# Performance work log

Measured on AMD Instinct MI355X. Metric: run time of the kernel, lower is better.

Reference implementation:

```python
import jax, jax.numpy as jnp
import numpy as np

V, E, H, C, M, CLS = 32000, 300, 512, 256, 512, 1
B, T = 64, 128
NEG = -1e9


def setup_inputs() -> dict:
    key = jax.random.key(0)
    ks = jax.random.split(key, 16)
    u = lambda k, shape, r: jax.random.uniform(k, shape, jnp.float32, -r, r)
    klstm = 1.0 / np.sqrt(H)
    inp = {
        "s1": jax.random.randint(ks[0], (B, T), 0, V, dtype=jnp.int32),
        "s2": jax.random.randint(ks[1], (B, T), 0, V, dtype=jnp.int32),
        "s1_length": jax.random.randint(ks[2], (B,), 1, T + 1, dtype=jnp.int32),
        "s2_length": jax.random.randint(ks[3], (B,), 1, T + 1, dtype=jnp.int32),
        "s1_h0": jnp.zeros((2, B, H), jnp.float32),
        "s1_c0": jnp.zeros((2, B, H), jnp.float32),
        "s2_h0": jnp.zeros((2, B, H), jnp.float32),
        "s2_c0": jnp.zeros((2, B, H), jnp.float32),
        "emb": jax.random.normal(ks[4], (V, E), jnp.float32) * 0.1,
        "Wih_f": u(ks[5], (4 * H, E), klstm),
        "Whh_f": u(ks[6], (4 * H, H), klstm),
        "b_f": u(ks[7], (4 * H,), klstm),
        "Wih_b": u(ks[8], (4 * H, E), klstm),
        "Whh_b": u(ks[9], (4 * H, H), klstm),
        "b_b": u(ks[10], (4 * H,), klstm),
        "S1W": u(ks[11], (C, 2 * H), 0.1),
        "S2W": u(ks[12], (1, C), 0.1),
        "mlpW": u(ks[13], (M, 4 * H), 0.1),
        "mlpb": jnp.zeros((M,), jnp.float32),
        "outW": u(ks[14], (CLS, M), 0.1),
        "outb": jnp.zeros((CLS,), jnp.float32),
    }
    return inp


def lstm(x, h0, c0, Wih, Whh, b):
    # x: [B,T,E] -> outputs [B,T,H]; PyTorch gate order i,f,g,o
    xW = jnp.einsum("bte,ge->btg", x, Wih) + b  # [B,T,4H]

    def step(carry, xw):
        h, c = carry
        g = xw + h @ Whh.T
        i, f, gg, o = jnp.split(g, 4, axis=-1)
        c = jax.nn.sigmoid(f) * c + jax.nn.sigmoid(i) * jnp.tanh(gg)
        h = jax.nn.sigmoid(o) * jnp.tanh(c)
        return (h, c), h

    _, hs = jax.lax.scan(step, (h0, c0), jnp.swapaxes(xW, 0, 1))
    return jnp.swapaxes(hs, 0, 1)


def encode(tokens, lens, h0, c0, emb, Wih_f, Whh_f, b_f, Wih_b, Whh_b, b_b, S1W, S2W):
    x = emb[tokens]  # [B,T,E]
    t = jnp.arange(tokens.shape[1])
    # reverse-within-valid-length indices (pack/pad semantics for bwd direction)
    idx = jnp.where(t[None, :] < lens[:, None], lens[:, None] - 1 - t[None, :], t[None, :])
    out_f = lstm(x, h0[0], c0[0], Wih_f, Whh_f, b_f)
    x_rev = jnp.take_along_axis(x, idx[:, :, None], axis=1)
    out_b = lstm(x_rev, h0[1], c0[1], Wih_b, Whh_b, b_b)
    out_b = jnp.take_along_axis(out_b, idx[:, :, None], axis=1)
    Hout = jnp.concatenate([out_f, out_b], axis=-1)  # [B,T,2H]
    # attention pooling: S2(tanh(S1(H))), softmax over valid positions
    scores = jnp.einsum("btc,c->bt", jnp.tanh(jnp.einsum("btd,cd->btc", Hout, S1W)), S2W[0])
    scores = jnp.where(t[None, :] < lens[:, None], scores, NEG)
    attn = jax.nn.softmax(scores, axis=1)
    return jnp.einsum("bt,btd->bd", attn, Hout)  # [B,2H]


def reference(s1, s2, s1_length, s2_length, s1_h0, s1_c0, s2_h0, s2_c0, emb,
              Wih_f, Whh_f, b_f, Wih_b, Whh_b, b_b, S1W, S2W, mlpW, mlpb, outW, outb):
    r1 = encode(s1, s1_length, s1_h0, s1_c0, emb, Wih_f, Whh_f, b_f, Wih_b, Whh_b, b_b, S1W, S2W)
    r2 = encode(s2, s2_length, s2_h0, s2_c0, emb, Wih_f, Whh_f, b_f, Wih_b, Whh_b, b_b, S1W, S2W)
    merged = jnp.concatenate([r1 + r2, (r1 - r2) ** 2], axis=1)  # [B,4H]
    out_mlp = merged @ mlpW.T + mlpb  # no activation, per original
    return jax.nn.sigmoid(out_mlp @ outW.T + outb)  # [B,CLS]
```

## Files before the change

kernel.cpp:

```cpp
#include <hip/hip_runtime.h>
#include <hip/hip_bf16.h>

#define B_  64
#define T_  128
#define E_  300
#define EP  320
#define H_  512
#define G4  2048
#define R_  128
#define C_  256
#define M_  512
#define TS  (T_ + 1)
#define NB  128
#define SENT 0xFFFFFFFFFFFFFFFFULL

typedef short bf16x8 __attribute__((ext_vector_type(8)));
typedef float f32x4  __attribute__((ext_vector_type(4)));
#define MFMA(a, b, c) __builtin_amdgcn_mfma_f32_16x16x32_bf16((a), (b), (c), 0, 0, 0)

__device__ __forceinline__ float fsig(float x) { return 1.0f / (1.0f + __expf(-x)); }
__device__ __forceinline__ float ftanh(float x) {
    float a = fminf(fabsf(x), 15.0f);
    float e = __expf(2.0f * a);
    return copysignf((e - 1.0f) / (e + 1.0f), x);
}
__device__ __forceinline__ ushort f2bf(float f) {
    __hip_bfloat16 h = __float2bfloat16(f);
    return *reinterpret_cast<ushort*>(&h);
}
__device__ __forceinline__ float bf2f(ushort u) {
    __hip_bfloat16 h = *reinterpret_cast<__hip_bfloat16*>(&u);
    return __bfloat162float(h);
}

__global__ __launch_bounds__(256) void k_cvt_all(
    const float* __restrict__ emb,
    const float* __restrict__ Wih_f, const float* __restrict__ Wih_b,
    const float* __restrict__ Whh_f, const float* __restrict__ Whh_b,
    const float* __restrict__ S1W,
    const float* __restrict__ s1_h0, const float* __restrict__ s2_h0,
    ushort* __restrict__ embB,
    ushort* __restrict__ WihBf, ushort* __restrict__ WihBb,
    ushort* __restrict__ WhhBf, ushort* __restrict__ WhhBb,
    ushort* __restrict__ S1WB,
    ushort* __restrict__ hfB, ushort* __restrict__ hbB)
{
    int b = blockIdx.x;
    if (b >= 40448) {
        const int r = b - 40448;
        const int rl = (r < B_) ? r : r - B_;
        const float* h0 = (r < B_) ? s1_h0 : s2_h0;
        for (int j = threadIdx.x; j < H_; j += 256) {
            hfB[(long)r * TS * H_ + j] = f2bf(h0[(long)0 * B_ * H_ + (long)rl * H_ + j]);
            hbB[(long)r * TS * H_ + j] = f2bf(h0[(long)1 * B_ * H_ + (long)rl * H_ + j]);
        }
        return;
    }
    const float* src; ushort* dst; int r, sk, dk;
    if (b < 32000)      { src = emb;   dst = embB;  r = b;          sk = E_;    dk = EP; }
    else if (b < 34048) { src = Wih_f; dst = WihBf; r = b - 32000;  sk = E_;    dk = EP; }
    else if (b < 36096) { src = Wih_b; dst = WihBb; r = b - 34048;  sk = E_;    dk = EP; }
    else if (b < 38144) { src = Whh_f; dst = WhhBf; r = b - 36096;  sk = H_;    dk = H_; }
    else if (b < 40192) { src = Whh_b; dst = WhhBb; r = b - 38144;  sk = H_;    dk = H_; }
    else                { src = S1W;   dst = S1WB;  r = b - 40192;  sk = 2*H_;  dk = 2*H_; }
    for (int c = threadIdx.x; c < dk; c += 256)
        dst[(long)r * dk + c] = (c < sk) ? f2bf(src[(long)r * sk + c]) : (ushort)0;
}

__global__ __launch_bounds__(256) void k_embed_mfma(
    const int* __restrict__ s1, const int* __restrict__ s2,
    const int* __restrict__ l1, const int* __restrict__ l2,
    const ushort* __restrict__ embB,
    const ushort* __restrict__ WihBf, const ushort* __restrict__ WihBb,
    const float* __restrict__ b_f, const float* __restrict__ b_b,
    ushort* __restrict__ xf, ushort* __restrict__ xb)
{
    const int dir = blockIdx.z;
    const int r   = blockIdx.y >> 1;
    const int t0  = (blockIdx.y & 1) * 64;
    const int N0  = blockIdx.x * 128;
    const int L   = (r < B_) ? l1[r] : l2[r - B_];
    if (L <= t0) return;

    const int tid = threadIdx.x;
    const int lane = tid & 63, w = tid >> 6;
    const int wm = w & 1, wn = w >> 1;
    const int l15 = lane & 15, q8 = (lane >> 4) * 8;

    __shared__ int toks[64];
    __shared__ __align__(16) ushort As[64][40];
    __shared__ __align__(16) ushort Bs[128][40];

    if (tid < 64) {
        int t  = t0 + tid;
        int tt = dir ? ((t < L) ? (L - 1 - t) : t) : t;
        toks[tid] = (r < B_) ? s1[r * T_ + tt] : s2[(r - B_) * T_ + tt];
    }
    __syncthreads();

    const ushort* Wih  = dir ? WihBb : WihBf;
    const float*  bias = dir ? b_b : b_f;

    f32x4 acc[2][4] = {};

    for (int k0 = 0; k0 < EP; k0 += 32) {
        {
            int row = tid >> 2, seg = tid & 3;
            *(uint4*)&As[row][seg * 8] =
                *(const uint4*)&embB[(long)toks[row] * EP + k0 + seg * 8];
        }
#pragma unroll
        for (int p = 0; p < 2; ++p) {
            int u = tid + p * 256;
            int row = u >> 2, seg = u & 3;
            *(uint4*)&Bs[row][seg * 8] =
                *(const uint4*)&Wih[(long)(N0 + row) * EP + k0 + seg * 8];
        }
        __syncthreads();
        bf16x8 af[2], bfr[4];
#pragma unroll
        for (int mt = 0; mt < 2; ++mt)
            af[mt] = *(const bf16x8*)&As[wm * 32 + mt * 16 + l15][q8];
#pragma unroll
        for (int nt = 0; nt < 4; ++nt)
            bfr[nt] = *(const bf16x8*)&Bs[wn * 64 + nt * 16 + l15][q8];
#pragma unroll
        for (int mt = 0; mt < 2; ++mt)
#pragma unroll
            for (int nt = 0; nt < 4; ++nt)
                acc[mt][nt] = MFMA(af[mt], bfr[nt], acc[mt][nt]);
        __syncthreads();
    }

    ushort* xout = dir ? xb : xf;
#pragma unroll
    for (int mt = 0; mt < 2; ++mt) {
        int m = r * T_ + t0 + wm * 32 + mt * 16 + (lane >> 4) * 4;
#pragma unroll
        for (int nt = 0; nt < 4; ++nt) {
            int col = N0 + wn * 64 + nt * 16 + l15;
            float bv = bias[col];
#pragma unroll
            for (int rg = 0; rg < 4; ++rg) {
                uint v = f2bf(acc[mt][nt][rg] + bv);
                uint pv = (uint)__shfl_xor((int)v, 1);
                if (!(lane & 1))
                    *(uint*)&xout[(long)(m + rg) * G4 + col] = v | (pv << 16);
            }
        }
    }
}

__global__ __launch_bounds__(256) void k_recur(
    const ushort* __restrict__ xf, const ushort* __restrict__ xb,
    ushort* __restrict__ hfB, ushort* __restrict__ hbB,
    const ushort* __restrict__ WhhBf, const ushort* __restrict__ WhhBb,
    const float* __restrict__ s1_c0, const float* __restrict__ s2_c0)
{
    const int bx = blockIdx.x;
    const int s  = bx >> 6;
    const int rb = (bx >> 4) & 3;
    const int jb = bx & 15;
    const int r0 = rb * 32, j0 = jb * 32;

    const ushort* xW  = s ? xb : xf;
    const ushort* Whh = s ? WhhBb : WhhBf;
    ushort* hB = s ? hbB : hfB;

    const int tid = threadIdx.x;
    const int lane = tid & 63;
    const int g = tid >> 6;
    const int l15 = lane & 15, q8 = (lane >> 4) * 8;

    __shared__ __align__(16) ushort As[32][520];
    __shared__ float Gs[4][32][33];

    bf16x8 bfr[2][16];
#pragma unroll
    for (int nt = 0; nt < 2; ++nt) {
        const ushort* brow = &Whh[((long)g * H_ + j0 + nt * 16 + l15) * H_];
#pragma unroll
        for (int ks = 0; ks < 16; ++ks)
            bfr[nt][ks] = *(const bf16x8*)&brow[ks * 32 + q8];
    }

    const int rr = tid >> 3, jj = (tid & 7) * 4;
    const int rg_ = r0 + rr;
    const int rl  = (rg_ < B_) ? rg_ : rg_ - B_;
    const float* c0p = (rg_ < B_) ? s1_c0 : s2_c0;
    float cst[4];
#pragma unroll
    for (int cc = 0; cc < 4; ++cc)
        cst[cc] = c0p[(long)s * B_ * H_ + (long)rl * H_ + j0 + jj + cc];

    const int arow = tid >> 3, aseg = tid & 7;
    const int swz = ((aseg + arow) & 7) * 8;

    for (int t = 0; t < T_; ++t) {
        uint2 xw[4];
        const long xbase = ((long)rg_ * T_ + t) * G4 + j0 + jj;
#pragma unroll
        for (int gg = 0; gg < 4; ++gg)
            xw[gg] = *(const uint2*)&xW[xbase + gg * H_];

        const ushort* hrow = &hB[((long)(r0 + arow) * TS + t) * H_ + aseg * 8];
        unsigned long long hv[16];
        bool ok;
        do {
#pragma unroll
            for (int i = 0; i < 16; ++i) {
                const unsigned long long* p8 =
                    (const unsigned long long*)(hrow + (i >> 1) * 64 + (i & 1) * 4);
                hv[i] = __hip_atomic_load(p8, __ATOMIC_RELAXED,
                                          __HIP_MEMORY_SCOPE_AGENT);
            }
            ok = true;
#pragma unroll
            for (int i = 0; i < 16; ++i)
                ok = ok && (hv[i] != SENT);
        } while (!ok);

#pragma unroll
        for (int sl = 0; sl < 8; ++sl) {
            uint4 av;
            av.x = (uint)hv[2 * sl];       av.y = (uint)(hv[2 * sl] >> 32);
            av.z = (uint)hv[2 * sl + 1];   av.w = (uint)(hv[2 * sl + 1] >> 32);
            *(uint4*)&As[arow][sl * 64 + swz] = av;
        }
        __syncthreads();

        f32x4 acc[2][2] = {};
#pragma unroll
        for (int ks = 0; ks < 16; ++ks) {
            const int e  = ks * 32 + q8;
            const int sl = e >> 6;
            const int c  = (e >> 3) & 7;
            bf16x8 a0 = *(const bf16x8*)&As[l15][sl * 64 + (((c + l15) & 7) << 3)];
            bf16x8 a1 = *(const bf16x8*)&As[16 + l15][sl * 64 + (((c + l15) & 7) << 3)];
            acc[0][0] = MFMA(a0, bfr[0][ks], acc[0][0]);
            acc[0][1] = MFMA(a0, bfr[1][ks], acc[0][1]);
            acc[1][0] = MFMA(a1, bfr[0][ks], acc[1][0]);
            acc[1][1] = MFMA(a1, bfr[1][ks], acc[1][1]);
        }

#pragma unroll
        for (int mt = 0; mt < 2; ++mt)
#pragma unroll
            for (int nt = 0; nt < 2; ++nt)
#pragma unroll
                for (int rg2 = 0; rg2 < 4; ++rg2)
                    Gs[g][mt * 16 + (lane >> 4) * 4 + rg2][nt * 16 + l15] =
                        acc[mt][nt][rg2];
        __syncthreads();

        ushort hp[4];
#pragma unroll
        for (int cc = 0; cc < 4; ++cc) {
            uint xv0 = (cc < 2) ? xw[0].x : xw[0].y;
            uint xv1 = (cc < 2) ? xw[1].x : xw[1].y;
            uint xv2 = (cc < 2) ? xw[2].x : xw[2].y;
            uint xv3 = (cc < 2) ? xw[3].x : xw[3].y;
            int sh = (cc & 1) * 16;
            float gi = Gs[0][rr][jj + cc] + bf2f((ushort)(xv0 >> sh));
            float gf = Gs[1][rr][jj + cc] + bf2f((ushort)(xv1 >> sh));
            float gg = Gs[2][rr][jj + cc] + bf2f((ushort)(xv2 >> sh));
            float go = Gs[3][rr][jj + cc] + bf2f((ushort)(xv3 >> sh));
            cst[cc] = fsig(gf) * cst[cc] + fsig(gi) * ftanh(gg);
            hp[cc] = f2bf(fsig(go) * ftanh(cst[cc]));
        }
        unsigned long long pk = (unsigned long long)hp[0]
                              | ((unsigned long long)hp[1] << 16)
                              | ((unsigned long long)hp[2] << 32)
                              | ((unsigned long long)hp[3] << 48);
        __hip_atomic_store(
            (unsigned long long*)&hB[((long)rg_ * TS + t + 1) * H_ + j0 + jj],
            pk, __ATOMIC_RELAXED, __HIP_MEMORY_SCOPE_AGENT);
    }
}

__global__ __launch_bounds__(256) void k_attn_mfma(
    const ushort* __restrict__ hfB, const ushort* __restrict__ hbB,
    const int* __restrict__ l1, const int* __restrict__ l2,
    const ushort* __restrict__ S1WB, float* __restrict__ U)
{
    const int r  = blockIdx.y >> 1;
    const int t0 = (blockIdx.y & 1) * 64;
    const int N0 = blockIdx.x * 64;
    const int L  = (r < B_) ? l1[r] : l2[r - B_];
    if (L <= t0) return;

    const int tid = threadIdx.x;
    const int lane = tid & 63, w = tid >> 6;
    const int wm = w & 1, wn = w >> 1;
    const int l15 = lane & 15, q8 = (lane >> 4) * 8;

    __shared__ __align__(16) ushort As[64][72];
    __shared__ __align__(16) ushort Bs[64][72];

    f32x4 acc[2][2] = {};

    for (int k0 = 0; k0 < 2 * H_; k0 += 64) {
#pragma unroll
        for (int p = 0; p < 2; ++p) {
            int u = tid + p * 256;
            int row = u >> 3, seg = u & 7;
            int tpos = t0 + row;
            int k = k0 + seg * 8;
            long idx;
            const ushort* src;
            if (k0 < H_) {
                src = hfB; idx = ((long)r * TS + tpos + 1) * H_ + k;
            } else {
                int tt = (tpos < L) ? (L - 1 - tpos) : tpos;
                src = hbB; idx = ((long)r * TS + tt + 1) * H_ + (k - H_);
            }
            *(uint4*)&As[row][seg * 8] = *(const uint4*)&src[idx];
        }
#pragma unroll
        for (int p = 0; p < 2; ++p) {
            int u = tid + p * 256;
            int row = u >> 3, seg = u & 7;
            *(uint4*)&Bs[row][seg * 8] =
                *(const uint4*)&S1WB[(long)(N0 + row) * (2 * H_) + k0 + seg * 8];
        }
        __syncthreads();
#pragma unroll
        for (int ks = 0; ks < 2; ++ks) {
            bf16x8 a0 = *(const bf16x8*)&As[wm * 32 + l15][ks * 32 + q8];
            bf16x8 a1 = *(const bf16x8*)&As[wm * 32 + 16 + l15][ks * 32 + q8];
            bf16x8 b0 = *(const bf16x8*)&Bs[wn * 32 + l15][ks * 32 + q8];
            bf16x8 b1 = *(const bf16x8*)&Bs[wn * 32 + 16 + l15][ks * 32 + q8];
            acc[0][0] = MFMA(a0, b0, acc[0][0]);
            acc[0][1] = MFMA(a0, b1, acc[0][1]);
            acc[1][0] = MFMA(a1, b0, acc[1][0]);
            acc[1][1] = MFMA(a1, b1, acc[1][1]);
        }
        __syncthreads();
    }
#pragma unroll
    for (int mt = 0; mt < 2; ++mt) {
        int m = r * T_ + t0 + wm * 32 + mt * 16 + (lane >> 4) * 4;
#pragma unroll
        for (int nt = 0; nt < 2; ++nt) {
            int col = N0 + wn * 32 + nt * 16 + l15;
#pragma unroll
            for (int rg = 0; rg < 4; ++rg)
                U[(long)(m + rg) * C_ + col] = ftanh(acc[mt][nt][rg]);
        }
    }
}

__global__ __launch_bounds__(256) void k_attn_pool(
    const ushort* __restrict__ hfB, const ushort* __restrict__ hbB,
    const float* __restrict__ U, const float* __restrict__ S2W,
    const int* __restrict__ l1, const int* __restrict__ l2,
    float* __restrict__ pooled)
{
    const int r = blockIdx.x;
    const int L = (r < B_) ? l1[r] : l2[r - B_];
    const int tid = threadIdx.x;
    const int lane = tid & 63, w = tid >> 6;

    __shared__ float att[T_];

    for (int tt = w; tt < T_; tt += 4) {
        float p = 0.0f;
        if (tt < L) {
            const float* u = &U[(long)(r * T_ + tt) * C_];
            p = u[lane] * S2W[lane] + u[lane + 64] * S2W[lane + 64]
              + u[lane + 128] * S2W[lane + 128] + u[lane + 192] * S2W[lane + 192];
            for (int off = 32; off; off >>= 1) p += __shfl_down(p, off);
        }
        if (lane == 0) att[tt] = p;
    }
    __syncthreads();

    float mx = -1e30f;
    for (int tt = 0; tt < L; ++tt) mx = fmaxf(mx, att[tt]);
    __syncthreads();
    if (tid < T_) att[tid] = (tid < L) ? __expf(att[tid] - mx) : 0.0f;
    __syncthreads();
    float sum = 0.0f;
    for (int tt = 0; tt < L; ++tt) sum += att[tt];
    float inv = 1.0f / sum;

    for (int p = tid; p < 512; p += 256) {
        float a0 = 0.0f, a1 = 0.0f;
        if (p < 256) {
            int d = p * 2;
            for (int tt = 0; tt < L; ++tt) {
                uint hv = *(const uint*)&hfB[((long)r * TS + tt + 1) * H_ + d];
                a0 += att[tt] * bf2f((ushort)(hv & 0xffff));
                a1 += att[tt] * bf2f((ushort)(hv >> 16));
            }
            pooled[(long)r * (2 * H_) + d]     = a0 * inv;
            pooled[(long)r * (2 * H_) + d + 1] = a1 * inv;
        } else {
            int d = (p - 256) * 2;
            for (int tt = 0; tt < L; ++tt) {
                uint hv = *(const uint*)&hbB[((long)r * TS + (L - tt)) * H_ + d];
                a0 += att[tt] * bf2f((ushort)(hv & 0xffff));
                a1 += att[tt] * bf2f((ushort)(hv >> 16));
            }
            pooled[(long)r * (2 * H_) + H_ + d]     = a0 * inv;
            pooled[(long)r * (2 * H_) + H_ + d + 1] = a1 * inv;
        }
    }
}

__global__ __launch_bounds__(256) void k_mlp1(
    const float* __restrict__ pooled,
    const float* __restrict__ mlpW, const float* __restrict__ mlpb,
    float* __restrict__ om)
{
    const int mg = blockIdx.x;
    const int b  = blockIdx.y;
    const int tid = threadIdx.x;
    const int lane = tid & 63, w = tid >> 6;

    __shared__ __align__(16) float sm[2048];

#pragma unroll
    for (int it = 0; it < 8; ++it) {
        int d = tid + it * 256;
        float v;
        if (d < 1024) {
            v = pooled[(long)b * 1024 + d] + pooled[(long)(B_ + b) * 1024 + d];
        } else {
            int dd = d - 1024;
            float x = pooled[(long)b * 1024 + dd] - pooled[(long)(B_ + b) * 1024 + dd];
            v = x * x;
        }
        sm[d] = v;
    }
    __syncthreads();

    for (int i = 0; i < 16; ++i) {
        int mm = mg * 64 + w * 16 + i;
        const float* wrow = &mlpW[(long)mm * 2048];
        float ax = 0.f, ay = 0.f, az = 0.f, aw = 0.f;
#pragma unroll
        for (int it = 0; it < 8; ++it) {
            int k = it * 256 + lane * 4;
            float4 wv = *(const float4*)&wrow[k];
            float4 sv = *(const float4*)&sm[k];
            ax += wv.x * sv.x; ay += wv.y * sv.y;
            az += wv.z * sv.z; aw += wv.w * sv.w;
        }
        float ssum = (ax + ay) + (az + aw);
        for (int off = 32; off; off >>= 1) ssum += __shfl_down(ssum, off);
        if (lane == 0) om[(long)b * M_ + mm] = ssum + mlpb[mm];
    }
}

__global__ __launch_bounds__(256) void k_final(
    const float* __restrict__ om,
    const float* __restrict__ outW, const float* __restrict__ outb,
    float* __restrict__ out)
{
    const int b = blockIdx.x;
    const int tid = threadIdx.x;
    __shared__ float red[256];
    float p = om[(long)b * M_ + tid] * outW[tid]
            + om[(long)b * M_ + 256 + tid] * outW[256 + tid];
    red[tid] = p;
    __syncthreads();
    for (int off = 128; off > 0; off >>= 1) {
        if (tid < off) red[tid] += red[tid + off];
        __syncthreads();
    }
    if (tid == 0) out[b] = 1.0f / (1.0f + __expf(-(red[0] + outb[0])));
}

extern "C" void kernel_launch(void* const* d_in, const int* in_sizes, int n_in,
                              void* d_out, int out_size, void* d_ws, size_t ws_size,
                              hipStream_t stream)
{
    const int*   s1    = (const int*)d_in[0];
    const int*   s2    = (const int*)d_in[1];
    const int*   l1    = (const int*)d_in[2];
    const int*   l2    = (const int*)d_in[3];
    const float* s1_h0 = (const float*)d_in[4];
    const float* s1_c0 = (const float*)d_in[5];
    const float* s2_h0 = (const float*)d_in[6];
    const float* s2_c0 = (const float*)d_in[7];
    const float* emb   = (const float*)d_in[8];
    const float* Wih_f = (const float*)d_in[9];
    const float* Whh_f = (const float*)d_in[10];
    const float* b_f   = (const float*)d_in[11];
    const float* Wih_b = (const float*)d_in[12];
    const float* Whh_b = (const float*)d_in[13];
    const float* b_b   = (const float*)d_in[14];
    const float* S1W   = (const float*)d_in[15];
    const float* S2W   = (const float*)d_in[16];
    const float* mlpW  = (const float*)d_in[17];
    const float* mlpb  = (const float*)d_in[18];
    const float* outW  = (const float*)d_in[19];
    const float* outb  = (const float*)d_in[20];
    float* out = (float*)d_out;

    ushort* p16 = (ushort*)d_ws;
    ushort* embB  = p16;  p16 += (long)32000 * EP;
    ushort* WihBf = p16;  p16 += (long)G4 * EP;
    ushort* WihBb = p16;  p16 += (long)G4 * EP;
    ushort* WhhBf = p16;  p16 += (long)G4 * H_;
    ushort* WhhBb = p16;  p16 += (long)G4 * H_;
    ushort* S1WB  = p16;  p16 += (long)C_ * 2 * H_;
    ushort* xf    = p16;  p16 += (long)R_ * T_ * G4;
    ushort* xb    = p16;  p16 += (long)R_ * T_ * G4;
    ushort* hfB   = p16;  p16 += (long)R_ * TS * H_;
    ushort* hbB   = p16;  p16 += (long)R_ * TS * H_;
    float* pf = (float*)p16;
    float* U      = pf;   pf += (long)R_ * T_ * C_;
    float* pooled = pf;   pf += (long)R_ * 2 * H_;
    float* om     = pf;   pf += (long)B_ * M_;

    hipMemsetAsync(hfB, 0xFF, (size_t)2 * R_ * TS * H_ * sizeof(ushort), stream);

    k_cvt_all<<<40576, 256, 0, stream>>>(emb, Wih_f, Wih_b, Whh_f, Whh_b, S1W,
                                         s1_h0, s2_h0,
                                         embB, WihBf, WihBb, WhhBf, WhhBb, S1WB,
                                         hfB, hbB);

    k_embed_mfma<<<dim3(16, 256, 2), 256, 0, stream>>>(
        s1, s2, l1, l2, embB, WihBf, WihBb, b_f, b_b, xf, xb);

    k_recur<<<NB, 256, 0, stream>>>(xf, xb, hfB, hbB, WhhBf, WhhBb,
                                    s1_c0, s2_c0);

    k_attn_mfma<<<dim3(4, 256), 256, 0, stream>>>(hfB, hbB, l1, l2, S1WB, U);
    k_attn_pool<<<R_, 256, 0, stream>>>(hfB, hbB, U, S2W, l1, l2, pooled);

    k_mlp1<<<dim3(8, B_), 256, 0, stream>>>(pooled, mlpW, mlpb, om);
    k_final<<<B_, 256, 0, stream>>>(om, outW, outb, out);
}
```

Measured before the change: 801.1 us.

## Convert embeddings and Whh on the fly; halve recurrence blocks with 512 threads

The full 32000x300 embedding table and the Whh matrices are no longer pre-converted to bf16 in a separate pass. Embedding rows are converted while loading inside the input-projection GEMM, and Whh is converted into registers at the start of the recurrence kernel. The recurrence now runs 64 blocks of 512 threads, each covering 64 hidden columns, and the spin-wait polls h-chunks independently with a pending mask. This removes a large conversion kernel and halves the number of blocks that must synchronise each step, at the cost of more per-block work per timestep.

```diff
diff --git a/kernel.cpp b/kernel.cpp
--- a/kernel.cpp
+++ b/kernel.cpp
@@ -11,7 +11,7 @@
 #define C_  256
 #define M_  512
 #define TS  (T_ + 1)
-#define NB  128
+#define NB2 64
 #define SENT 0xFFFFFFFFFFFFFFFFULL
 
 typedef short bf16x8 __attribute__((ext_vector_type(8)));
@@ -34,20 +34,16 @@
 }
 
 __global__ __launch_bounds__(256) void k_cvt_all(
-    const float* __restrict__ emb,
     const float* __restrict__ Wih_f, const float* __restrict__ Wih_b,
-    const float* __restrict__ Whh_f, const float* __restrict__ Whh_b,
     const float* __restrict__ S1W,
     const float* __restrict__ s1_h0, const float* __restrict__ s2_h0,
-    ushort* __restrict__ embB,
     ushort* __restrict__ WihBf, ushort* __restrict__ WihBb,
-    ushort* __restrict__ WhhBf, ushort* __restrict__ WhhBb,
     ushort* __restrict__ S1WB,
     ushort* __restrict__ hfB, ushort* __restrict__ hbB)
 {
     int b = blockIdx.x;
-    if (b >= 40448) {
-        const int r = b - 40448;
+    if (b >= 4352) {
+        const int r = b - 4352;
         const int rl = (r < B_) ? r : r - B_;
         const float* h0 = (r < B_) ? s1_h0 : s2_h0;
         for (int j = threadIdx.x; j < H_; j += 256) {
@@ -57,12 +53,9 @@
         return;
     }
     const float* src; ushort* dst; int r, sk, dk;
-    if (b < 32000)      { src = emb;   dst = embB;  r = b;          sk = E_;    dk = EP; }
-    else if (b < 34048) { src = Wih_f; dst = WihBf; r = b - 32000;  sk = E_;    dk = EP; }
-    else if (b < 36096) { src = Wih_b; dst = WihBb; r = b - 34048;  sk = E_;    dk = EP; }
-    else if (b < 38144) { src = Whh_f; dst = WhhBf; r = b - 36096;  sk = H_;    dk = H_; }
-    else if (b < 40192) { src = Whh_b; dst = WhhBb; r = b - 38144;  sk = H_;    dk = H_; }
-    else                { src = S1W;   dst = S1WB;  r = b - 40192;  sk = 2*H_;  dk = 2*H_; }
+    if (b < 2048)      { src = Wih_f; dst = WihBf; r = b;         sk = E_;    dk = EP; }
+    else if (b < 4096) { src = Wih_b; dst = WihBb; r = b - 2048;  sk = E_;    dk = EP; }
+    else               { src = S1W;   dst = S1WB;  r = b - 4096;  sk = 2*H_;  dk = 2*H_; }
     for (int c = threadIdx.x; c < dk; c += 256)
         dst[(long)r * dk + c] = (c < sk) ? f2bf(src[(long)r * sk + c]) : (ushort)0;
 }
@@ -70,7 +63,7 @@
 __global__ __launch_bounds__(256) void k_embed_mfma(
     const int* __restrict__ s1, const int* __restrict__ s2,
     const int* __restrict__ l1, const int* __restrict__ l2,
-    const ushort* __restrict__ embB,
+    const float* __restrict__ emb,
     const ushort* __restrict__ WihBf, const ushort* __restrict__ WihBb,
     const float* __restrict__ b_f, const float* __restrict__ b_b,
     ushort* __restrict__ xf, ushort* __restrict__ xb)
@@ -106,8 +99,24 @@
     for (int k0 = 0; k0 < EP; k0 += 32) {
         {
             int row = tid >> 2, seg = tid & 3;
-            *(uint4*)&As[row][seg * 8] =
-                *(const uint4*)&embB[(long)toks[row] * EP + k0 + seg * 8];
+            int kb = k0 + seg * 8;
+            const float* er = &emb[(long)toks[row] * E_];
+            bf16x8 v;
+            if (kb + 8 <= E_) {
+                float4 f0 = *(const float4*)&er[kb];
+                float4 f1 = *(const float4*)&er[kb + 4];
+                v[0] = (short)f2bf(f0.x); v[1] = (short)f2bf(f0.y);
+                v[2] = (short)f2bf(f0.z); v[3] = (short)f2bf(f0.w);
+                v[4] = (short)f2bf(f1.x); v[5] = (short)f2bf(f1.y);
+                v[6] = (short)f2bf(f1.z); v[7] = (short)f2bf(f1.w);
+            } else {
+#pragma unroll
+                for (int e = 0; e < 8; ++e) {
+                    int k = kb + e;
+                    v[e] = (k < E_) ? (short)f2bf(er[k]) : (short)0;
+                }
+            }
+            *(bf16x8*)&As[row][seg * 8] = v;
         }
 #pragma unroll
         for (int p = 0; p < 2; ++p) {
@@ -151,40 +160,51 @@
     }
 }
 
-__global__ __launch_bounds__(256) void k_recur(
+__global__ __launch_bounds__(512, 2) void k_recur(
     const ushort* __restrict__ xf, const ushort* __restrict__ xb,
     ushort* __restrict__ hfB, ushort* __restrict__ hbB,
-    const ushort* __restrict__ WhhBf, const ushort* __restrict__ WhhBb,
+    const float* __restrict__ Whh_f, const float* __restrict__ Whh_b,
     const float* __restrict__ s1_c0, const float* __restrict__ s2_c0)
 {
     const int bx = blockIdx.x;
-    const int s  = bx >> 6;
-    const int rb = (bx >> 4) & 3;
-    const int jb = bx & 15;
-    const int r0 = rb * 32, j0 = jb * 32;
+    const int g7 = bx & 7;
+    const int s  = g7 >> 2;
+    const int rb = g7 & 3;
+    const int jb = bx >> 3;
+    const int r0 = rb * 32, j0 = jb * 64;
 
     const ushort* xW  = s ? xb : xf;
-    const ushort* Whh = s ? WhhBb : WhhBf;
+    const float*  Whh = s ? Whh_b : Whh_f;
     ushort* hB = s ? hbB : hfB;
 
-    const int tid = threadIdx.x;
+    const int tid  = threadIdx.x;
     const int lane = tid & 63;
-    const int g = tid >> 6;
+    const int w    = tid >> 6;
+    const int g    = w & 3;
+    const int nh   = w >> 2;
     const int l15 = lane & 15, q8 = (lane >> 4) * 8;
 
     __shared__ __align__(16) ushort As[32][520];
-    __shared__ float Gs[4][32][33];
+    __shared__ float Gs[4][32][65];
 
     bf16x8 bfr[2][16];
 #pragma unroll
     for (int nt = 0; nt < 2; ++nt) {
-        const ushort* brow = &Whh[((long)g * H_ + j0 + nt * 16 + l15) * H_];
-#pragma unroll
-        for (int ks = 0; ks < 16; ++ks)
-            bfr[nt][ks] = *(const bf16x8*)&brow[ks * 32 + q8];
-    }
-
-    const int rr = tid >> 3, jj = (tid & 7) * 4;
+        const float* brow = &Whh[((long)g * H_ + j0 + nh * 32 + nt * 16 + l15) * H_];
+#pragma unroll
+        for (int ks = 0; ks < 16; ++ks) {
+            float4 f0 = *(const float4*)&brow[ks * 32 + q8];
+            float4 f1 = *(const float4*)&brow[ks * 32 + q8 + 4];
+            bf16x8 v;
+            v[0] = (short)f2bf(f0.x); v[1] = (short)f2bf(f0.y);
+            v[2] = (short)f2bf(f0.z); v[3] = (short)f2bf(f0.w);
+            v[4] = (short)f2bf(f1.x); v[5] = (short)f2bf(f1.y);
+            v[6] = (short)f2bf(f1.z); v[7] = (short)f2bf(f1.w);
+            bfr[nt][ks] = v;
+        }
+    }
+
+    const int rr = tid >> 4, jj = (tid & 15) * 4;
     const int rg_ = r0 + rr;
     const int rl  = (rg_ < B_) ? rg_ : rg_ - B_;
     const float* c0p = (rg_ < B_) ? s1_c0 : s2_c0;
@@ -193,8 +213,8 @@
     for (int cc = 0; cc < 4; ++cc)
         cst[cc] = c0p[(long)s * B_ * H_ + (long)rl * H_ + j0 + jj + cc];
 
-    const int arow = tid >> 3, aseg = tid & 7;
-    const int swz = ((aseg + arow) & 7) * 8;
+    const int arow = tid >> 4, hs = tid & 15;
+    const int cch = hs & 7, sb = (hs >> 3) * 4;
 
     for (int t = 0; t < T_; ++t) {
         uint2 xw[4];
@@ -203,30 +223,30 @@
         for (int gg = 0; gg < 4; ++gg)
             xw[gg] = *(const uint2*)&xW[xbase + gg * H_];
 
-        const ushort* hrow = &hB[((long)(r0 + arow) * TS + t) * H_ + aseg * 8];
-        unsigned long long hv[16];
-        bool ok;
+        const ushort* hrow = &hB[((long)(r0 + arow) * TS + t) * H_];
+        uint pend = 0xF;
         do {
-#pragma unroll
-            for (int i = 0; i < 16; ++i) {
-                const unsigned long long* p8 =
-                    (const unsigned long long*)(hrow + (i >> 1) * 64 + (i & 1) * 4);
-                hv[i] = __hip_atomic_load(p8, __ATOMIC_RELAXED,
-                                          __HIP_MEMORY_SCOPE_AGENT);
-            }
-            ok = true;
-#pragma unroll
-            for (int i = 0; i < 16; ++i)
-                ok = ok && (hv[i] != SENT);
-        } while (!ok);
-
-#pragma unroll
-        for (int sl = 0; sl < 8; ++sl) {
-            uint4 av;
-            av.x = (uint)hv[2 * sl];       av.y = (uint)(hv[2 * sl] >> 32);
-            av.z = (uint)hv[2 * sl + 1];   av.w = (uint)(hv[2 * sl + 1] >> 32);
-            *(uint4*)&As[arow][sl * 64 + swz] = av;
-        }
+            unsigned long long lo[4], hi[4];
+#pragma unroll
+            for (int s2 = 0; s2 < 4; ++s2)
+                if (pend & (1u << s2)) {
+                    const unsigned long long* p8 = (const unsigned long long*)
+                        (hrow + (sb + s2) * 64 + cch * 8);
+                    lo[s2] = __hip_atomic_load(p8,     __ATOMIC_RELAXED,
+                                               __HIP_MEMORY_SCOPE_AGENT);
+                    hi[s2] = __hip_atomic_load(p8 + 1, __ATOMIC_RELAXED,
+                                               __HIP_MEMORY_SCOPE_AGENT);
+                }
+#pragma unroll
+            for (int s2 = 0; s2 < 4; ++s2)
+                if ((pend & (1u << s2)) && lo[s2] != SENT && hi[s2] != SENT) {
+                    uint4 av;
+                    av.x = (uint)lo[s2]; av.y = (uint)(lo[s2] >> 32);
+                    av.z = (uint)hi[s2]; av.w = (uint)(hi[s2] >> 32);
+                    *(uint4*)&As[arow][(sb + s2) * 64 + (((cch + arow) & 7) << 3)] = av;
+                    pend &= ~(1u << s2);
+                }
+        } while (pend);
         __syncthreads();
 
         f32x4 acc[2][2] = {};
@@ -249,7 +269,7 @@
             for (int nt = 0; nt < 2; ++nt)
 #pragma unroll
                 for (int rg2 = 0; rg2 < 4; ++rg2)
-                    Gs[g][mt * 16 + (lane >> 4) * 4 + rg2][nt * 16 + l15] =
+                    Gs[g][mt * 16 + (lane >> 4) * 4 + rg2][nh * 32 + nt * 16 + l15] =
                         acc[mt][nt][rg2];
         __syncthreads();
 
@@ -500,11 +520,8 @@
     float* out = (float*)d_out;
 
     ushort* p16 = (ushort*)d_ws;
-    ushort* embB  = p16;  p16 += (long)32000 * EP;
     ushort* WihBf = p16;  p16 += (long)G4 * EP;
     ushort* WihBb = p16;  p16 += (long)G4 * EP;
-    ushort* WhhBf = p16;  p16 += (long)G4 * H_;
-    ushort* WhhBb = p16;  p16 += (long)G4 * H_;
     ushort* S1WB  = p16;  p16 += (long)C_ * 2 * H_;
     ushort* xf    = p16;  p16 += (long)R_ * T_ * G4;
     ushort* xb    = p16;  p16 += (long)R_ * T_ * G4;
@@ -517,16 +534,14 @@
 
     hipMemsetAsync(hfB, 0xFF, (size_t)2 * R_ * TS * H_ * sizeof(ushort), stream);
 
-    k_cvt_all<<<40576, 256, 0, stream>>>(emb, Wih_f, Wih_b, Whh_f, Whh_b, S1W,
-                                         s1_h0, s2_h0,
-                                         embB, WihBf, WihBb, WhhBf, WhhBb, S1WB,
-                                         hfB, hbB);
+    k_cvt_all<<<4480, 256, 0, stream>>>(Wih_f, Wih_b, S1W, s1_h0, s2_h0,
+                                        WihBf, WihBb, S1WB, hfB, hbB);
 
     k_embed_mfma<<<dim3(16, 256, 2), 256, 0, stream>>>(
-        s1, s2, l1, l2, embB, WihBf, WihBb, b_f, b_b, xf, xb);
-
-    k_recur<<<NB, 256, 0, stream>>>(xf, xb, hfB, hbB, WhhBf, WhhBb,
-                                    s1_c0, s2_c0);
+        s1, s2, l1, l2, emb, WihBf, WihBb, b_f, b_b, xf, xb);
+
+    k_recur<<<NB2, 512, 0, stream>>>(xf, xb, hfB, hbB, Whh_f, Whh_b,
+                                     s1_c0, s2_c0);
 
     k_attn_mfma<<<dim3(4, 256), 256, 0, stream>>>(hfB, hbB, l1, l2, S1WB, U);
     k_attn_pool<<<R_, 256, 0, stream>>>(hfB, hbB, U, S2W, l1, l2, pooled);
```

After: 974.4 us. 21.6% more time.

## Fuse attention score GEMM with pooling and widen embedding GEMM tiles

Applied to the files above, without the earlier changes.

The attention projection GEMM, tanh, S2 dot product, softmax and pooling are merged into one kernel per row. Each block computes the full 128x256 score tile in registers and reduces it into shared memory, so the U buffer is no longer written and read back through global memory. Separately, the embedding input-projection GEMM uses 256-wide N tiles with 64-deep K steps to cut loop iterations and redundant A loads. In exchange, the fused kernel launches only 128 blocks with heavy register use (128 accumulators per thread) and can no longer skip padded time tiles.

```diff
diff --git a/kernel.cpp b/kernel.cpp
--- a/kernel.cpp
+++ b/kernel.cpp
@@ -78,7 +78,7 @@
     const int dir = blockIdx.z;
     const int r   = blockIdx.y >> 1;
     const int t0  = (blockIdx.y & 1) * 64;
-    const int N0  = blockIdx.x * 128;
+    const int N0  = blockIdx.x * 256;
     const int L   = (r < B_) ? l1[r] : l2[r - B_];
     if (L <= t0) return;
 
@@ -88,8 +88,8 @@
     const int l15 = lane & 15, q8 = (lane >> 4) * 8;
 
     __shared__ int toks[64];
-    __shared__ __align__(16) ushort As[64][40];
-    __shared__ __align__(16) ushort Bs[128][40];
+    __shared__ __align__(16) ushort As[64][72];
+    __shared__ __align__(16) ushort Bs[256][72];
 
     if (tid < 64) {
         int t  = t0 + tid;
@@ -101,34 +101,39 @@
     const ushort* Wih  = dir ? WihBb : WihBf;
     const float*  bias = dir ? b_b : b_f;
 
-    f32x4 acc[2][4] = {};
-
-    for (int k0 = 0; k0 < EP; k0 += 32) {
-        {
-            int row = tid >> 2, seg = tid & 3;
+    f32x4 acc[2][8] = {};
+
+    for (int k0 = 0; k0 < EP; k0 += 64) {
+#pragma unroll
+        for (int p = 0; p < 2; ++p) {
+            int u = tid + p * 256;
+            int row = u >> 3, seg = u & 7;
             *(uint4*)&As[row][seg * 8] =
                 *(const uint4*)&embB[(long)toks[row] * EP + k0 + seg * 8];
         }
 #pragma unroll
-        for (int p = 0; p < 2; ++p) {
+        for (int p = 0; p < 8; ++p) {
             int u = tid + p * 256;
-            int row = u >> 2, seg = u & 3;
+            int row = u >> 3, seg = u & 7;
             *(uint4*)&Bs[row][seg * 8] =
                 *(const uint4*)&Wih[(long)(N0 + row) * EP + k0 + seg * 8];
         }
         __syncthreads();
-        bf16x8 af[2], bfr[4];
-#pragma unroll
-        for (int mt = 0; mt < 2; ++mt)
-            af[mt] = *(const bf16x8*)&As[wm * 32 + mt * 16 + l15][q8];
-#pragma unroll
-        for (int nt = 0; nt < 4; ++nt)
-            bfr[nt] = *(const bf16x8*)&Bs[wn * 64 + nt * 16 + l15][q8];
-#pragma unroll
-        for (int mt = 0; mt < 2; ++mt)
-#pragma unroll
-            for (int nt = 0; nt < 4; ++nt)
-                acc[mt][nt] = MFMA(af[mt], bfr[nt], acc[mt][nt]);
+#pragma unroll
+        for (int ks = 0; ks < 2; ++ks) {
+            bf16x8 af[2], bfr[8];
+#pragma unroll
+            for (int mt = 0; mt < 2; ++mt)
+                af[mt] = *(const bf16x8*)&As[wm * 32 + mt * 16 + l15][ks * 32 + q8];
+#pragma unroll
+            for (int nt = 0; nt < 8; ++nt)
+                bfr[nt] = *(const bf16x8*)&Bs[wn * 128 + nt * 16 + l15][ks * 32 + q8];
+#pragma unroll
+            for (int mt = 0; mt < 2; ++mt)
+#pragma unroll
+                for (int nt = 0; nt < 8; ++nt)
+                    acc[mt][nt] = MFMA(af[mt], bfr[nt], acc[mt][nt]);
+        }
         __syncthreads();
     }
 
@@ -137,8 +142,8 @@
     for (int mt = 0; mt < 2; ++mt) {
         int m = r * T_ + t0 + wm * 32 + mt * 16 + (lane >> 4) * 4;
 #pragma unroll
-        for (int nt = 0; nt < 4; ++nt) {
-            int col = N0 + wn * 64 + nt * 16 + l15;
+        for (int nt = 0; nt < 8; ++nt) {
+            int col = N0 + wn * 128 + nt * 16 + l15;
             float bv = bias[col];
 #pragma unroll
             for (int rg = 0; rg < 4; ++rg) {
@@ -278,107 +283,95 @@
     }
 }
 
-__global__ __launch_bounds__(256) void k_attn_mfma(
+__global__ __launch_bounds__(256) void k_attn_fused(
     const ushort* __restrict__ hfB, const ushort* __restrict__ hbB,
     const int* __restrict__ l1, const int* __restrict__ l2,
-    const ushort* __restrict__ S1WB, float* __restrict__ U)
-{
-    const int r  = blockIdx.y >> 1;
-    const int t0 = (blockIdx.y & 1) * 64;
-    const int N0 = blockIdx.x * 64;
-    const int L  = (r < B_) ? l1[r] : l2[r - B_];
-    if (L <= t0) return;
-
+    const ushort* __restrict__ S1WB, const float* __restrict__ S2W,
+    float* __restrict__ pooled)
+{
+    const int r = blockIdx.x;
+    const int L = (r < B_) ? l1[r] : l2[r - B_];
     const int tid = threadIdx.x;
     const int lane = tid & 63, w = tid >> 6;
     const int wm = w & 1, wn = w >> 1;
     const int l15 = lane & 15, q8 = (lane >> 4) * 8;
 
-    __shared__ __align__(16) ushort As[64][72];
-    __shared__ __align__(16) ushort Bs[64][72];
-
-    f32x4 acc[2][2] = {};
+    __shared__ __align__(16) ushort As[128][72];
+    __shared__ __align__(16) ushort Bs[256][72];
+    __shared__ float sc[T_];
+    __shared__ float att[T_];
+
+    if (tid < T_) sc[tid] = 0.0f;
+
+    f32x4 acc[4][8] = {};
 
     for (int k0 = 0; k0 < 2 * H_; k0 += 64) {
 #pragma unroll
-        for (int p = 0; p < 2; ++p) {
+        for (int p = 0; p < 4; ++p) {
             int u = tid + p * 256;
             int row = u >> 3, seg = u & 7;
-            int tpos = t0 + row;
             int k = k0 + seg * 8;
             long idx;
             const ushort* src;
             if (k0 < H_) {
-                src = hfB; idx = ((long)r * TS + tpos + 1) * H_ + k;
+                src = hfB; idx = ((long)r * TS + row + 1) * H_ + k;
             } else {
-                int tt = (tpos < L) ? (L - 1 - tpos) : tpos;
+                int tt = (row < L) ? (L - 1 - row) : row;
                 src = hbB; idx = ((long)r * TS + tt + 1) * H_ + (k - H_);
             }
             *(uint4*)&As[row][seg * 8] = *(const uint4*)&src[idx];
         }
 #pragma unroll
-        for (int p = 0; p < 2; ++p) {
+        for (int p = 0; p < 8; ++p) {
             int u = tid + p * 256;
             int row = u >> 3, seg = u & 7;
             *(uint4*)&Bs[row][seg * 8] =
-                *(const uint4*)&S1WB[(long)(N0 + row) * (2 * H_) + k0 + seg * 8];
+                *(const uint4*)&S1WB[(long)row * (2 * H_) + k0 + seg * 8];
         }
         __syncthreads();
 #pragma unroll
         for (int ks = 0; ks < 2; ++ks) {
-            bf16x8 a0 = *(const bf16x8*)&As[wm * 32 + l15][ks * 32 + q8];
-            bf16x8 a1 = *(const bf16x8*)&As[wm * 32 + 16 + l15][ks * 32 + q8];
-            bf16x8 b0 = *(const bf16x8*)&Bs[wn * 32 + l15][ks * 32 + q8];
-            bf16x8 b1 = *(const bf16x8*)&Bs[wn * 32 + 16 + l15][ks * 32 + q8];
-            acc[0][0] = MFMA(a0, b0, acc[0][0]);
-            acc[0][1] = MFMA(a0, b1, acc[0][1]);
-            acc[1][0] = MFMA(a1, b0, acc[1][0]);
-            acc[1][1] = MFMA(a1, b1, acc[1][1]);
-        }
-        __syncthreads();
-    }
-#pragma unroll
-    for (int mt = 0; mt < 2; ++mt) {
-        int m = r * T_ + t0 + wm * 32 + mt * 16 + (lane >> 4) * 4;
-#pragma unroll
-        for (int nt = 0; nt < 2; ++nt) {
-            int col = N0 + wn * 32 + nt * 16 + l15;
-#pragma unroll
-            for (int rg = 0; rg < 4; ++rg)
-                U[(long)(m + rg) * C_ + col] = ftanh(acc[mt][nt][rg]);
-        }
-    }
-}
-
-__global__ __launch_bounds__(256) void k_attn_pool(
-    const ushort* __restrict__ hfB, const ushort* __restrict__ hbB,
-    const float* __restrict__ U, const float* __restrict__ S2W,
-    const int* __restrict__ l1, const int* __restrict__ l2,
-    float* __restrict__ pooled)
-{
-    const int r = blockIdx.x;
-    const int L = (r < B_) ? l1[r] : l2[r - B_];
-    const int tid = threadIdx.x;
-    const int lane = tid & 63, w = tid >> 6;
-
-    __shared__ float att[T_];
-
-    for (int tt = w; tt < T_; tt += 4) {
-        float p = 0.0f;
-        if (tt < L) {
-            const float* u = &U[(long)(r * T_ + tt) * C_];
-            p = u[lane] * S2W[lane] + u[lane + 64] * S2W[lane + 64]
-              + u[lane + 128] * S2W[lane + 128] + u[lane + 192] * S2W[lane + 192];
-            for (int off = 32; off; off >>= 1) p += __shfl_down(p, off);
-        }
-        if (lane == 0) att[tt] = p;
-    }
+            bf16x8 af[4], bfr[8];
+#pragma unroll
+            for (int mt = 0; mt < 4; ++mt)
+                af[mt] = *(const bf16x8*)&As[wm * 64 + mt * 16 + l15][ks * 32 + q8];
+#pragma unroll
+            for (int nt = 0; nt < 8; ++nt)
+                bfr[nt] = *(const bf16x8*)&Bs[wn * 128 + nt * 16 + l15][ks * 32 + q8];
+#pragma unroll
+            for (int mt = 0; mt < 4; ++mt)
+#pragma unroll
+                for (int nt = 0; nt < 8; ++nt)
+                    acc[mt][nt] = MFMA(af[mt], bfr[nt], acc[mt][nt]);
+        }
+        __syncthreads();
+    }
+
+    float s2r[8];
+#pragma unroll
+    for (int nt = 0; nt < 8; ++nt)
+        s2r[nt] = S2W[wn * 128 + nt * 16 + l15];
+#pragma unroll
+    for (int mt = 0; mt < 4; ++mt)
+#pragma unroll
+        for (int rg = 0; rg < 4; ++rg) {
+            float v = 0.0f;
+#pragma unroll
+            for (int nt = 0; nt < 8; ++nt)
+                v += ftanh(acc[mt][nt][rg]) * s2r[nt];
+            v += __shfl_xor(v, 1);
+            v += __shfl_xor(v, 2);
+            v += __shfl_xor(v, 4);
+            v += __shfl_xor(v, 8);
+            if (l15 == 0)
+                atomicAdd(&sc[wm * 64 + mt * 16 + (lane >> 4) * 4 + rg], v);
+        }
     __syncthreads();
 
     float mx = -1e30f;
-    for (int tt = 0; tt < L; ++tt) mx = fmaxf(mx, att[tt]);
+    for (int tt = 0; tt < L; ++tt) mx = fmaxf(mx, sc[tt]);
     __syncthreads();
-    if (tid < T_) att[tid] = (tid < L) ? __expf(att[tid] - mx) : 0.0f;
+    if (tid < T_) att[tid] = (tid < L) ? __expf(sc[tid] - mx) : 0.0f;
     __syncthreads();
     float sum = 0.0f;
     for (int tt = 0; tt < L; ++tt) sum += att[tt];
@@ -511,7 +504,6 @@
     ushort* hfB   = p16;  p16 += (long)R_ * TS * H_;
     ushort* hbB   = p16;  p16 += (long)R_ * TS * H_;
     float* pf = (float*)p16;
-    float* U      = pf;   pf += (long)R_ * T_ * C_;
     float* pooled = pf;   pf += (long)R_ * 2 * H_;
     float* om     = pf;   pf += (long)B_ * M_;
 
@@ -522,14 +514,13 @@
                                          embB, WihBf, WihBb, WhhBf, WhhBb, S1WB,
                                          hfB, hbB);
 
-    k_embed_mfma<<<dim3(16, 256, 2), 256, 0, stream>>>(
+    k_embed_mfma<<<dim3(8, 256, 2), 256, 0, stream>>>(
         s1, s2, l1, l2, embB, WihBf, WihBb, b_f, b_b, xf, xb);
 
     k_recur<<<NB, 256, 0, stream>>>(xf, xb, hfB, hbB, WhhBf, WhhBb,
                                     s1_c0, s2_c0);
 
-    k_attn_mfma<<<dim3(4, 256), 256, 0, stream>>>(hfB, hbB, l1, l2, S1WB, U);
-    k_attn_pool<<<R_, 256, 0, stream>>>(hfB, hbB, U, S2W, l1, l2, pooled);
+    k_attn_fused<<<R_, 256, 0, stream>>>(hfB, hbB, l1, l2, S1WB, S2W, pooled);
 
     k_mlp1<<<dim3(8, B_), 256, 0, stream>>>(pooled, mlpW, mlpb, om);
     k_final<<<B_, 256, 0, stream>>>(om, outW, outb, out);
```

Measured after the change: 802.8 us. No clear change (+0.2%).
